# Kernel tuning notes

Measured on AMD Instinct MI355X. Metric: run time of the kernel, lower is better.

The kernel has to match this reference:

```python
import jax, jax.numpy as jnp
import numpy as np

B, C_IN, N = 64, 1, 8192
WIDTH, MODES, NLAYERS = 64, 16, 4


def setup_inputs() -> dict:
    key = jax.random.key(0)
    ks = jax.random.split(key, 10)
    scale = 1.0 / (WIDTH * WIDTH)
    inp = {
        "x": jax.random.normal(ks[0], (B, C_IN, N), dtype=jnp.float32),
        # lifting p: Linear(2, width)
        "p_w": jax.random.normal(ks[1], (WIDTH, 2), dtype=jnp.float32) * 0.5,
        "p_b": jax.random.normal(ks[2], (WIDTH,), dtype=jnp.float32) * 0.1,
        # 4 spectral conv weights, complex stored as real/imag (uniform like torch.rand cfloat)
        "sc_wr": scale * jax.random.uniform(ks[3], (NLAYERS, WIDTH, WIDTH, MODES), dtype=jnp.float32),
        "sc_wi": scale * jax.random.uniform(ks[4], (NLAYERS, WIDTH, WIDTH, MODES), dtype=jnp.float32),
        # 4 pointwise (1x1) conv weights/biases
        "w_w": jax.random.normal(ks[5], (NLAYERS, WIDTH, WIDTH), dtype=jnp.float32) / np.sqrt(WIDTH),
        "w_b": jax.random.normal(ks[6], (NLAYERS, WIDTH), dtype=jnp.float32) * 0.1,
        # projection q: Linear(width, 1)
        "q_w": jax.random.normal(ks[7], (1, WIDTH), dtype=jnp.float32) / np.sqrt(WIDTH),
        "q_b": jax.random.normal(ks[8], (1,), dtype=jnp.float32) * 0.1,
    }
    return inp


def spectral_conv(x, wr, wi, n):
    # x: [b, i, n] real; weights complex [i, o, modes]
    x_ft = jnp.fft.rfft(x, axis=-1)                      # [b, i, n//2+1] complex
    w = (wr + 1j * wi).astype(jnp.complex64)
    out_modes = jnp.einsum('bix,iox->box', x_ft[:, :, :MODES], w)
    out_ft = jnp.zeros((x.shape[0], w.shape[1], n // 2 + 1), dtype=jnp.complex64)
    out_ft = out_ft.at[:, :, :MODES].set(out_modes)
    return jnp.fft.irfft(out_ft, n=n, axis=-1)


def reference(x, p_w, p_b, sc_wr, sc_wi, w_w, w_b, q_w, q_b):
    b, _, n = x.shape
    grid = jnp.broadcast_to(jnp.linspace(0.0, 1.0, n, dtype=jnp.float32)[None, None, :], (b, 1, n))
    h = jnp.concatenate([x, grid], axis=1)               # [b, 2, n]
    # lifting: Linear over channel dim
    h = jnp.einsum('bcn,wc->bwn', h, p_w) + p_b[None, :, None]
    for l in range(NLAYERS):
        x1 = spectral_conv(h, sc_wr[l], sc_wi[l], n)
        x2 = jnp.einsum('bin,oi->bon', h, w_w[l]) + w_b[l][None, :, None]
        h = jax.nn.gelu(x1 + x2, approximate=False)
    out = jnp.einsum('bwn,ow->bon', h, q_w) + q_b[None, :, None]  # [b, 1, n]
    return out
```

## Files before the change

### kernel.cpp

```cpp
#include <hip/hip_runtime.h>
#include <math.h>


typedef _Float16 f16;
typedef _Float16 f16x2 __attribute__((ext_vector_type(2)));
typedef _Float16 f16x4 __attribute__((ext_vector_type(4)));
typedef _Float16 f16x8 __attribute__((ext_vector_type(8)));
typedef float    f32x2 __attribute__((ext_vector_type(2)));
typedef float    f32x4 __attribute__((ext_vector_type(4)));
typedef unsigned int u32;

#define BB 64
#define NN 8192

#define HT_S 64
#define HO_S 136
#define WS_S 72
#define MS_S 40
#define BI_S 40
#define BF_S 136

__device__ __forceinline__ int ht_swz(int n) { return ((n & 7) ^ ((n >> 3) & 7)) << 3; }

__device__ __forceinline__ float gelu_f(float v) {
    float x  = v * 0.70710678118654752f;
    float ax = fabsf(x);
    float t  = __builtin_amdgcn_rcpf(fmaf(0.3275911f, ax, 1.0f));
    float p  = fmaf(1.061405429f, t, -1.453152027f);
    p = fmaf(p, t, 1.421413741f);
    p = fmaf(p, t, -0.284496736f);
    p = fmaf(p, t, 0.254829592f);
    p = p * t;
    float e  = __expf(-x * x);
    float er = fmaf(-p, e, 1.0f);
    er = copysignf(er, x);
    return 0.5f * fmaf(v, er, v);
}

__global__ __launch_bounds__(256) void fill_basis(f16* __restrict__ basF,
                                                  f16* __restrict__ basI,
                                                  const float* __restrict__ w_w,
                                                  f16* __restrict__ Wh,
                                                  float* __restrict__ Sz) {
    int n = blockIdx.x * 256 + threadIdx.x;
    f16 row[32];
#pragma unroll
    for (int k = 0; k < 16; ++k) {
        float s, c;
        sincospif((float)(k * n) * (1.0f / 4096.0f), &s, &c);
        basF[k * NN + n]        = (f16)c;
        basF[(16 + k) * NN + n] = (f16)(-s);
        row[2 * k]     = (f16)c;
        row[2 * k + 1] = (f16)s;
    }
#pragma unroll
    for (int q = 0; q < 4; ++q) *(f16x8*)&basI[n * 32 + 8 * q] = *(f16x8*)&row[8 * q];
    Wh[n]        = (f16)w_w[n];
    Wh[n + 8192] = (f16)w_w[n + 8192];
    f32x4* S4 = (f32x4*)Sz;
    f32x4 z = {0.f, 0.f, 0.f, 0.f};
#pragma unroll
    for (int u = 0; u < 4; ++u) S4[n * 4 + u] = z;
}

__global__ __launch_bounds__(1024) void mode_mix(float* __restrict__ S,
                                                 const float* __restrict__ wr,
                                                 const float* __restrict__ wi,
                                                 f16* __restrict__ Mph) {
    int b = blockIdx.x, t = threadIdx.x;
    __shared__ float Ss[32 * 66];
    if (t < 512) {
        f32x4 v = *(const f32x4*)&S[b * 2048 + t * 4];
        int rw = t >> 4, cl = (t & 15) * 4;
#pragma unroll
        for (int e = 0; e < 4; ++e) Ss[rw * 66 + cl + e] = v[e];
    }
    __syncthreads();
    *(f32x2*)&S[b * 2048 + t * 2] = (f32x2){0.f, 0.f};

    int o = t >> 4, k = t & 15;
    const float* wrp = wr + o * 16 + k;
    const float* wip = wi + o * 16 + k;
    float ar = 0.f, ai = 0.f;
#pragma unroll 8
    for (int i = 0; i < 64; ++i) {
        float sr = Ss[k * 66 + i], si = Ss[(16 + k) * 66 + i];
        float wrv = wrp[i * 1024];
        float wiv = wip[i * 1024];
        ar = fmaf(sr, wrv, ar); ar = fmaf(-si, wiv, ar);
        ai = fmaf(sr, wiv, ai); ai = fmaf(si, wrv, ai);
    }
    float sc = (k == 0 ? 1.0f : 2.0f) * (1.0f / 8192.0f);
    f16x2 outv = { (f16)(sc * ar), (f16)(-sc * ai) };
    *(f16x2*)&Mph[b * 2048 + o * 32 + 2 * k] = outv;
}

__device__ __forceinline__ void dft_accum(const f16* Hout, const f16* BasF,
                                          f32x4 sacc[2], int lane, int wv) {
    int q = lane >> 4, l15 = lane & 15;
    int o = (wv << 4) + l15;
#pragma unroll
    for (int ks = 0; ks < 4; ++ks) {
        f16x8 bh = *(const f16x8*)&Hout[o * HO_S + ks * 32 + q * 8];
#pragma unroll
        for (int mt = 0; mt < 2; ++mt) {
            f16x8 af = *(const f16x8*)&BasF[(mt * 16 + l15) * BF_S + ks * 32 + q * 8];
            sacc[mt] = __builtin_amdgcn_mfma_f32_16x16x32_f16(af, bh, sacc[mt], 0, 0, 0);
        }
    }
}

__device__ __forceinline__ void dft_flush(const f32x4 sacc[2], float* __restrict__ S,
                                          int b, int lane, int wv) {
    int q = lane >> 4, l15 = lane & 15;
#pragma unroll
    for (int mt = 0; mt < 2; ++mt)
#pragma unroll
        for (int r = 0; r < 4; ++r)
            atomicAdd(&S[(b * 32 + mt * 16 + q * 4 + r) * 64 + (wv << 4) + l15],
                      sacc[mt][r]);
}

__global__ __launch_bounds__(256, 3) void lift_kernel(const float* __restrict__ x,
                                                      const float* __restrict__ p_w,
                                                      const float* __restrict__ p_b,
                                                      f16* __restrict__ h,
                                                      const f16* __restrict__ basF_g,
                                                      float* __restrict__ S) {
    __shared__ f16 Hout[64 * HO_S];
    __shared__ f16 BasF[32 * BF_S];
    int t = threadIdx.x;
    int b = blockIdx.x >> 5;
    int g = blockIdx.x & 31;
    int lane = t & 63, wv = t >> 6;
    int ns = (t & 15) << 3;

    float w0[4], w1[4], pb[4];
#pragma unroll
    for (int r = 0; r < 4; ++r) {
        int o = (t >> 4) + 16 * r;
        w0[r] = p_w[2 * o]; w1[r] = p_w[2 * o + 1]; pb[r] = p_b[o];
    }

    f32x4 X[2][2];
#pragma unroll
    for (int tile = 0; tile < 2; ++tile) {
        int n0 = ((g << 1) + tile) << 7;
        X[tile][0] = *(const f32x4*)&x[(b << 13) + n0 + ns];
        X[tile][1] = *(const f32x4*)&x[(b << 13) + n0 + ns + 4];
    }

    f32x4 sacc[2] = {{0.f,0.f,0.f,0.f},{0.f,0.f,0.f,0.f}};
#pragma unroll
    for (int tile = 0; tile < 2; ++tile) {
        int n0 = ((g << 1) + tile) << 7;
#pragma unroll
        for (int r = 0; r < 4; ++r) {
            int o = (t >> 4) + 16 * r;
            f16 vals[8];
#pragma unroll
            for (int j = 0; j < 8; ++j) {
                int n = n0 + ns + j;
                float xv = X[tile][j >> 2][j & 3];
                vals[j] = (f16)(w0[r] * xv + w1[r] * ((float)n * (1.0f / 8191.0f)) + pb[r]);
            }
            *(f16x8*)&Hout[o * HO_S + ns] = *(f16x8*)vals;
            *(f16x8*)(h + (((size_t)(b * 64 + o)) << 13) + n0 + ns) = *(f16x8*)vals;
        }
#pragma unroll
        for (int u = 0; u < 2; ++u) {
            int km = t >> 3, nn = (t & 7) * 16 + u * 8;
            *(f16x8*)&BasF[km * BF_S + nn] = *(const f16x8*)&basF_g[km * NN + n0 + nn];
        }
        __syncthreads();
        dft_accum(Hout, BasF, sacc, lane, wv);
        if (tile == 0) __syncthreads();
    }
    dft_flush(sacc, S, b, lane, wv);
}

template <int DO_DFT>
__global__ __launch_bounds__(256, 3) void layer_kernel(f16* __restrict__ h,
                                                       const f16* __restrict__ Wl_h,
                                                       const float* __restrict__ bl,
                                                       const f16* __restrict__ Mph,
                                                       const f16* __restrict__ basF_g,
                                                       const f16* __restrict__ basI_g,
                                                       float* __restrict__ S,
                                                       const float* __restrict__ q_w,
                                                       const float* __restrict__ q_b,
                                                       float* __restrict__ out) {
    __shared__ __align__(16) char pool[16384 + 9216];
    f16* Ht   = (f16*)pool;
    f16* Ws   = (f16*)(pool + 16384);
    f16* Hout = (f16*)pool;
    __shared__ f16 Ms2[64 * MS_S];
    __shared__ f16 BasI[128 * BI_S];
    __shared__ f16 BasF[32 * BF_S];
    __shared__ float bls[64];
    int t = threadIdx.x;
    int b = blockIdx.x >> 5;
    int g = blockIdx.x & 31;
    f16* hbase = h + (((size_t)(b * 64)) << 13);
    int lane = t & 63, wv = t >> 6;
    int q = lane >> 4, l15 = lane & 15;

    if (t >= 128) {
        int t2 = t - 128;
        {
            int o = t2 & 63, hs = (t2 >> 6) * 32;
            const f16* src = Wl_h + o * 64 + hs;
            f16* dst = &Ws[o * WS_S + hs];
#pragma unroll
            for (int u = 0; u < 4; ++u) *(f16x8*)&dst[8 * u] = *(const f16x8*)&src[8 * u];
        }
        {
            int o = t2 >> 1, seg = (t2 & 1) * 16;
            const f16* src = Mph + b * 2048 + o * 32 + seg;
            f16* dst = &Ms2[o * MS_S + seg];
            *(f16x8*)&dst[0] = *(const f16x8*)&src[0];
            *(f16x8*)&dst[8] = *(const f16x8*)&src[8];
        }
    }
    if (t < 64) bls[t] = bl[t];

    f16x8 Bw[4][2], Bm[4];
    f32x4 sacc[2] = {{0.f,0.f,0.f,0.f},{0.f,0.f,0.f,0.f}};

    for (int tile = 0; tile < 2; ++tile) {
        int n0 = ((g << 1) + tile) << 7;
        f16* hbt = hbase + n0;

        if (t < 128) {
            int ig = t >> 4, nb = t & 15;
            int i0 = ig << 3, ns = nb << 3;
            f16x8 R[8];
#pragma unroll
            for (int k = 0; k < 8; ++k)
                R[k] = *(const f16x8*)(hbt + ((size_t)(i0 + k) << 13) + ns);
            const u32* rd = (const u32*)R;
            int swz = nb & 7;
#pragma unroll
            for (int j = 0; j < 8; ++j) {
                u32 o[4] __attribute__((aligned(16)));
                u32 sel = (j & 1) ? 0x07060302u : 0x05040100u;
                int jd = j >> 1;
#pragma unroll
                for (int e = 0; e < 4; ++e)
                    o[e] = __builtin_amdgcn_perm(rd[(2 * e + 1) * 4 + jd],
                                                 rd[(2 * e) * 4 + jd], sel);
                int col = i0 ^ ((j ^ swz) << 3);
                *(f16x8*)&Ht[(ns + j) * HT_S + col] = *(const f16x8*)o;
            }
        } else {
            int t2 = t - 128;
            {
                const f16* src = basI_g + (size_t)(n0 + t2) * 32;
                f16* dst = &BasI[t2 * BI_S];
#pragma unroll
                for (int u = 0; u < 4; ++u) *(f16x8*)&dst[8 * u] = *(const f16x8*)&src[8 * u];
            }
            if (DO_DFT) {
                int km = t2 >> 2, seg = (t2 & 3) * 32;
                const f16* src = basF_g + km * NN + n0 + seg;
                f16* dst = &BasF[km * BF_S + seg];
#pragma unroll
                for (int u = 0; u < 4; ++u) *(f16x8*)&dst[8 * u] = *(const f16x8*)&src[8 * u];
            }
        }
        __syncthreads();

        if (tile == 0) {
#pragma unroll
            for (int ct = 0; ct < 4; ++ct) {
#pragma unroll
                for (int ks = 0; ks < 2; ++ks)
                    Bw[ct][ks] = *(const f16x8*)&Ws[(ct * 16 + l15) * WS_S + ks * 32 + q * 8];
                Bm[ct] = *(const f16x8*)&Ms2[(ct * 16 + l15) * MS_S + q * 8];
            }
        }

        f32x4 acc[4][2];
#pragma unroll
        for (int ct = 0; ct < 4; ++ct)
#pragma unroll
            for (int m = 0; m < 2; ++m) acc[ct][m] = (f32x4){0.f, 0.f, 0.f, 0.f};

#pragma unroll
        for (int mtl = 0; mtl < 2; ++mtl) {
            int nrow = (2 * wv + mtl) * 16 + l15;
            const f16* hrow = &Ht[nrow * HT_S];
            int g3 = ht_swz(nrow);
#pragma unroll
            for (int ks = 0; ks < 2; ++ks) {
                f16x8 Ah = *(const f16x8*)&hrow[(ks * 32 + q * 8) ^ g3];
#pragma unroll
                for (int ct = 0; ct < 4; ++ct)
                    acc[ct][mtl] = __builtin_amdgcn_mfma_f32_16x16x32_f16(
                        Ah, Bw[ct][ks], acc[ct][mtl], 0, 0, 0);
            }
            f16x8 Ab = *(const f16x8*)&BasI[nrow * BI_S + q * 8];
#pragma unroll
            for (int ct = 0; ct < 4; ++ct)
                acc[ct][mtl] = __builtin_amdgcn_mfma_f32_16x16x32_f16(
                    Ab, Bm[ct], acc[ct][mtl], 0, 0, 0);
        }

        float bv[4];
#pragma unroll
        for (int ct = 0; ct < 4; ++ct) bv[ct] = bls[ct * 16 + l15];

        if (DO_DFT) {
            __syncthreads();
#pragma unroll
            for (int ct = 0; ct < 4; ++ct) {
                int o = ct * 16 + l15;
#pragma unroll
                for (int mtl = 0; mtl < 2; ++mtl) {
                    int nbase = (2 * wv + mtl) * 16 + q * 4;
                    float gg[4];
#pragma unroll
                    for (int r = 0; r < 4; ++r)
                        gg[r] = gelu_f(acc[ct][mtl][r] + bv[ct]);
                    f16x2 lo = __builtin_bit_cast(f16x2, __builtin_amdgcn_cvt_pkrtz(gg[0], gg[1]));
                    f16x2 hi = __builtin_bit_cast(f16x2, __builtin_amdgcn_cvt_pkrtz(gg[2], gg[3]));
                    f16x4 pk = {lo[0], lo[1], hi[0], hi[1]};
                    *(f16x4*)&Hout[o * HO_S + nbase] = pk;
                }
            }
            __syncthreads();
#pragma unroll
            for (int r = 0; r < 4; ++r) {
                int o = (t >> 4) + 16 * r;
                int ns2 = (t & 15) << 3;
                *(f16x8*)(hbt + ((size_t)o << 13) + ns2) = *(f16x8*)&Hout[o * HO_S + ns2];
            }
            dft_accum(Hout, BasF, sacc, lane, wv);
        } else {
            float qv[4];
#pragma unroll
            for (int ct = 0; ct < 4; ++ct) qv[ct] = q_w[ct * 16 + l15];
            float part[2][4] = {{0.f,0.f,0.f,0.f},{0.f,0.f,0.f,0.f}};
#pragma unroll
            for (int ct = 0; ct < 4; ++ct)
#pragma unroll
                for (int mtl = 0; mtl < 2; ++mtl)
#pragma unroll
                    for (int r = 0; r < 4; ++r)
                        part[mtl][r] = fmaf(qv[ct],
                            gelu_f(acc[ct][mtl][r] + bv[ct]), part[mtl][r]);
#pragma unroll
            for (int mtl = 0; mtl < 2; ++mtl)
#pragma unroll
                for (int r = 0; r < 4; ++r) {
                    float s = part[mtl][r];
#pragma unroll
                    for (int m = 1; m < 16; m <<= 1)
                        s += __shfl_xor(s, m, 64);
                    if (l15 == 0)
                        out[(b << 13) + n0 + (2 * wv + mtl) * 16 + q * 4 + r] =
                            s + q_b[0];
                }
        }
        if (tile == 0) __syncthreads();
    }
    if (DO_DFT) dft_flush(sacc, S, b, lane, wv);
}

extern "C" void kernel_launch(void* const* d_in, const int* in_sizes, int n_in,
                              void* d_out, int out_size, void* d_ws, size_t ws_size,
                              hipStream_t stream) {
    const float* x     = (const float*)d_in[0];
    const float* p_w   = (const float*)d_in[1];
    const float* p_b   = (const float*)d_in[2];
    const float* sc_wr = (const float*)d_in[3];
    const float* sc_wi = (const float*)d_in[4];
    const float* w_w   = (const float*)d_in[5];
    const float* w_b   = (const float*)d_in[6];
    const float* q_w   = (const float*)d_in[7];
    const float* q_b   = (const float*)d_in[8];
    float* out = (float*)d_out;

    char* ws = (char*)d_ws;
    f16*   h    = (f16*)ws;
    float* S    = (float*)(ws + 67108864ull);
    f16*   Mph  = (f16*)(ws + 67633152ull);
    f16*   basF = (f16*)(ws + 67895296ull);
    f16*   basI = (f16*)(ws + 68419584ull);
    f16*   Wh   = (f16*)(ws + 68943872ull);

    hipLaunchKernelGGL(fill_basis, dim3(NN / 256), dim3(256), 0, stream,
                       basF, basI, w_w, Wh, S);
    hipLaunchKernelGGL(lift_kernel, dim3(BB * 32), dim3(256), 0, stream,
                       x, p_w, p_b, h, basF, S);
    for (int l = 0; l < 4; ++l) {
        hipLaunchKernelGGL(mode_mix, dim3(BB), dim3(1024), 0, stream,
                           S, sc_wr + l * 65536, sc_wi + l * 65536, Mph);
        if (l < 3) {
            hipLaunchKernelGGL((layer_kernel<1>), dim3(BB * 32), dim3(256), 0, stream,
                               h, Wh + l * 4096, w_b + l * 64, Mph, basF, basI, S,
                               q_w, q_b, out);
        } else {
            hipLaunchKernelGGL((layer_kernel<0>), dim3(BB * 32), dim3(256), 0, stream,
                               h, Wh + l * 4096, w_b + l * 64, Mph, basF, basI, S,
                               q_w, q_b, out);
        }
    }
}
```

Baseline: 267.1 us.

## Software-pipeline layer tiles, drop basis/weight LDS staging, read fragments from global

Restructures the layer kernel into an explicitly unrolled two-tile pipeline. The second tile's h rows and inverse-basis fragments are prefetched into registers while the first tile computes, and all 256 threads now share the transpose. Weights, spectral mode coefficients and DFT basis fragments are loaded directly from global memory into MFMA operands instead of being staged through shared memory, which shrinks LDS use and removes barriers. The risks are higher register pressure under launch_bounds(256,3) and uncoalesced global fragment loads that depend on cache hits.

```diff
diff --git a/kernel.cpp b/kernel.cpp
--- a/kernel.cpp
+++ b/kernel.cpp
@@ -15,10 +15,6 @@
 
 #define HT_S 64
 #define HO_S 136
-#define WS_S 72
-#define MS_S 40
-#define BI_S 40
-#define BF_S 136
 
 __device__ __forceinline__ int ht_swz(int n) { return ((n & 7) ^ ((n >> 3) & 7)) << 3; }
 
@@ -95,8 +91,8 @@
     *(f16x2*)&Mph[b * 2048 + o * 32 + 2 * k] = outv;
 }
 
-__device__ __forceinline__ void dft_accum(const f16* Hout, const f16* BasF,
-                                          f32x4 sacc[2], int lane, int wv) {
+__device__ __forceinline__ void dft_accum_g(const f16* Hout, const f16* __restrict__ basF_g,
+                                            int n0, f32x4 sacc[2], int lane, int wv) {
     int q = lane >> 4, l15 = lane & 15;
     int o = (wv << 4) + l15;
 #pragma unroll
@@ -104,7 +100,7 @@
         f16x8 bh = *(const f16x8*)&Hout[o * HO_S + ks * 32 + q * 8];
 #pragma unroll
         for (int mt = 0; mt < 2; ++mt) {
-            f16x8 af = *(const f16x8*)&BasF[(mt * 16 + l15) * BF_S + ks * 32 + q * 8];
+            f16x8 af = *(const f16x8*)&basF_g[(mt * 16 + l15) * NN + n0 + ks * 32 + q * 8];
             sacc[mt] = __builtin_amdgcn_mfma_f32_16x16x32_f16(af, bh, sacc[mt], 0, 0, 0);
         }
     }
@@ -128,7 +124,6 @@
                                                       const f16* __restrict__ basF_g,
                                                       float* __restrict__ S) {
     __shared__ f16 Hout[64 * HO_S];
-    __shared__ f16 BasF[32 * BF_S];
     int t = threadIdx.x;
     int b = blockIdx.x >> 5;
     int g = blockIdx.x & 31;
@@ -167,13 +162,8 @@
             *(f16x8*)&Hout[o * HO_S + ns] = *(f16x8*)vals;
             *(f16x8*)(h + (((size_t)(b * 64 + o)) << 13) + n0 + ns) = *(f16x8*)vals;
         }
-#pragma unroll
-        for (int u = 0; u < 2; ++u) {
-            int km = t >> 3, nn = (t & 7) * 16 + u * 8;
-            *(f16x8*)&BasF[km * BF_S + nn] = *(const f16x8*)&basF_g[km * NN + n0 + nn];
-        }
-        __syncthreads();
-        dft_accum(Hout, BasF, sacc, lane, wv);
+        __syncthreads();
+        dft_accum_g(Hout, basF_g, n0, sacc, lane, wv);
         if (tile == 0) __syncthreads();
     }
     dft_flush(sacc, S, b, lane, wv);
@@ -190,13 +180,8 @@
                                                        const float* __restrict__ q_w,
                                                        const float* __restrict__ q_b,
                                                        float* __restrict__ out) {
-    __shared__ __align__(16) char pool[16384 + 9216];
-    f16* Ht   = (f16*)pool;
-    f16* Ws   = (f16*)(pool + 16384);
-    f16* Hout = (f16*)pool;
-    __shared__ f16 Ms2[64 * MS_S];
-    __shared__ f16 BasI[128 * BI_S];
-    __shared__ f16 BasF[32 * BF_S];
+    __shared__ __align__(16) f16 Ht[128 * HT_S];
+    __shared__ __align__(16) f16 Hout[DO_DFT ? 64 * HO_S : 8];
     __shared__ float bls[64];
     int t = threadIdx.x;
     int b = blockIdx.x >> 5;
@@ -204,167 +189,236 @@
     f16* hbase = h + (((size_t)(b * 64)) << 13);
     int lane = t & 63, wv = t >> 6;
     int q = lane >> 4, l15 = lane & 15;
-
-    if (t >= 128) {
-        int t2 = t - 128;
+    int blk = t >> 1, half = t & 1;
+    int ig = blk >> 4, nb = blk & 15;
+    int i0 = ig << 3, nst = nb << 3;
+    int swz = nb & 7;
+    int n0_0 = (g << 1) << 7, n0_1 = ((g << 1) + 1) << 7;
+    f16* hbt0 = hbase + n0_0;
+    f16* hbt1 = hbase + n0_1;
+
+    f16x8 Bw[4][2], Bm[4];
+#pragma unroll
+    for (int ct = 0; ct < 4; ++ct) {
+#pragma unroll
+        for (int ks = 0; ks < 2; ++ks)
+            Bw[ct][ks] = *(const f16x8*)&Wl_h[(ct * 16 + l15) * 64 + ks * 32 + q * 8];
+        Bm[ct] = *(const f16x8*)&Mph[b * 2048 + (ct * 16 + l15) * 32 + q * 8];
+    }
+    if (t < 64) bls[t] = bl[t];
+
+    f16x8 R0[4];
+#pragma unroll
+    for (int k = 0; k < 4; ++k)
+        R0[k] = *(const f16x8*)(hbt0 + ((size_t)(i0 + half * 4 + k) << 13) + nst);
+    f16x8 Ab0[2];
+#pragma unroll
+    for (int mtl = 0; mtl < 2; ++mtl)
+        Ab0[mtl] = *(const f16x8*)&basI_g[(size_t)(n0_0 + (2 * wv + mtl) * 16 + l15) * 32 + q * 8];
+    {
+        const u32* rd = (const u32*)R0;
+#pragma unroll
+        for (int j = 0; j < 8; ++j) {
+            u32 sel = (j & 1) ? 0x07060302u : 0x05040100u;
+            int jd = j >> 1;
+            u32 oo[2] __attribute__((aligned(8)));
+            oo[0] = __builtin_amdgcn_perm(rd[4 + jd],  rd[jd],      sel);
+            oo[1] = __builtin_amdgcn_perm(rd[12 + jd], rd[8 + jd],  sel);
+            int col = (i0 ^ ((j ^ swz) << 3)) + half * 4;
+            *(f16x4*)&Ht[(nst + j) * HT_S + col] = *(const f16x4*)oo;
+        }
+    }
+    __syncthreads();
+
+    f16x8 R1[4];
+#pragma unroll
+    for (int k = 0; k < 4; ++k)
+        R1[k] = *(const f16x8*)(hbt1 + ((size_t)(i0 + half * 4 + k) << 13) + nst);
+    f16x8 Ab1[2];
+#pragma unroll
+    for (int mtl = 0; mtl < 2; ++mtl)
+        Ab1[mtl] = *(const f16x8*)&basI_g[(size_t)(n0_1 + (2 * wv + mtl) * 16 + l15) * 32 + q * 8];
+
+    float bv[4];
+#pragma unroll
+    for (int ct = 0; ct < 4; ++ct) bv[ct] = bls[ct * 16 + l15];
+
+    f32x4 sacc[2] = {{0.f,0.f,0.f,0.f},{0.f,0.f,0.f,0.f}};
+
+    f32x4 acc[4][2];
+#pragma unroll
+    for (int ct = 0; ct < 4; ++ct)
+#pragma unroll
+        for (int m = 0; m < 2; ++m) acc[ct][m] = (f32x4){0.f, 0.f, 0.f, 0.f};
+#pragma unroll
+    for (int mtl = 0; mtl < 2; ++mtl) {
+        int nrow = (2 * wv + mtl) * 16 + l15;
+        const f16* hrow = &Ht[nrow * HT_S];
+        int g3 = ht_swz(nrow);
+#pragma unroll
+        for (int ks = 0; ks < 2; ++ks) {
+            f16x8 Ah = *(const f16x8*)&hrow[(ks * 32 + q * 8) ^ g3];
+#pragma unroll
+            for (int ct = 0; ct < 4; ++ct)
+                acc[ct][mtl] = __builtin_amdgcn_mfma_f32_16x16x32_f16(
+                    Ah, Bw[ct][ks], acc[ct][mtl], 0, 0, 0);
+        }
+#pragma unroll
+        for (int ct = 0; ct < 4; ++ct)
+            acc[ct][mtl] = __builtin_amdgcn_mfma_f32_16x16x32_f16(
+                Ab0[mtl], Bm[ct], acc[ct][mtl], 0, 0, 0);
+    }
+
+    if (DO_DFT) {
+#pragma unroll
+        for (int ct = 0; ct < 4; ++ct) {
+            int o = ct * 16 + l15;
+#pragma unroll
+            for (int mtl = 0; mtl < 2; ++mtl) {
+                int nbase = (2 * wv + mtl) * 16 + q * 4;
+                float gg[4];
+#pragma unroll
+                for (int r = 0; r < 4; ++r)
+                    gg[r] = gelu_f(acc[ct][mtl][r] + bv[ct]);
+                f16x2 lo = __builtin_bit_cast(f16x2, __builtin_amdgcn_cvt_pkrtz(gg[0], gg[1]));
+                f16x2 hi = __builtin_bit_cast(f16x2, __builtin_amdgcn_cvt_pkrtz(gg[2], gg[3]));
+                f16x4 pk = {lo[0], lo[1], hi[0], hi[1]};
+                *(f16x4*)&Hout[o * HO_S + nbase] = pk;
+            }
+        }
+        __syncthreads();
+#pragma unroll
+        for (int r = 0; r < 4; ++r) {
+            int o = (t >> 4) + 16 * r;
+            int ns2 = (t & 15) << 3;
+            *(f16x8*)(hbt0 + ((size_t)o << 13) + ns2) = *(f16x8*)&Hout[o * HO_S + ns2];
+        }
         {
-            int o = t2 & 63, hs = (t2 >> 6) * 32;
-            const f16* src = Wl_h + o * 64 + hs;
-            f16* dst = &Ws[o * WS_S + hs];
-#pragma unroll
-            for (int u = 0; u < 4; ++u) *(f16x8*)&dst[8 * u] = *(const f16x8*)&src[8 * u];
-        }
-        {
-            int o = t2 >> 1, seg = (t2 & 1) * 16;
-            const f16* src = Mph + b * 2048 + o * 32 + seg;
-            f16* dst = &Ms2[o * MS_S + seg];
-            *(f16x8*)&dst[0] = *(const f16x8*)&src[0];
-            *(f16x8*)&dst[8] = *(const f16x8*)&src[8];
-        }
-    }
-    if (t < 64) bls[t] = bl[t];
-
-    f16x8 Bw[4][2], Bm[4];
-    f32x4 sacc[2] = {{0.f,0.f,0.f,0.f},{0.f,0.f,0.f,0.f}};
-
-    for (int tile = 0; tile < 2; ++tile) {
-        int n0 = ((g << 1) + tile) << 7;
-        f16* hbt = hbase + n0;
-
-        if (t < 128) {
-            int ig = t >> 4, nb = t & 15;
-            int i0 = ig << 3, ns = nb << 3;
-            f16x8 R[8];
-#pragma unroll
-            for (int k = 0; k < 8; ++k)
-                R[k] = *(const f16x8*)(hbt + ((size_t)(i0 + k) << 13) + ns);
-            const u32* rd = (const u32*)R;
-            int swz = nb & 7;
+            const u32* rd = (const u32*)R1;
 #pragma unroll
             for (int j = 0; j < 8; ++j) {
-                u32 o[4] __attribute__((aligned(16)));
                 u32 sel = (j & 1) ? 0x07060302u : 0x05040100u;
                 int jd = j >> 1;
-#pragma unroll
-                for (int e = 0; e < 4; ++e)
-                    o[e] = __builtin_amdgcn_perm(rd[(2 * e + 1) * 4 + jd],
-                                                 rd[(2 * e) * 4 + jd], sel);
-                int col = i0 ^ ((j ^ swz) << 3);
-                *(f16x8*)&Ht[(ns + j) * HT_S + col] = *(const f16x8*)o;
-            }
-        } else {
-            int t2 = t - 128;
-            {
-                const f16* src = basI_g + (size_t)(n0 + t2) * 32;
-                f16* dst = &BasI[t2 * BI_S];
-#pragma unroll
-                for (int u = 0; u < 4; ++u) *(f16x8*)&dst[8 * u] = *(const f16x8*)&src[8 * u];
-            }
-            if (DO_DFT) {
-                int km = t2 >> 2, seg = (t2 & 3) * 32;
-                const f16* src = basF_g + km * NN + n0 + seg;
-                f16* dst = &BasF[km * BF_S + seg];
-#pragma unroll
-                for (int u = 0; u < 4; ++u) *(f16x8*)&dst[8 * u] = *(const f16x8*)&src[8 * u];
-            }
-        }
-        __syncthreads();
-
-        if (tile == 0) {
-#pragma unroll
-            for (int ct = 0; ct < 4; ++ct) {
-#pragma unroll
-                for (int ks = 0; ks < 2; ++ks)
-                    Bw[ct][ks] = *(const f16x8*)&Ws[(ct * 16 + l15) * WS_S + ks * 32 + q * 8];
-                Bm[ct] = *(const f16x8*)&Ms2[(ct * 16 + l15) * MS_S + q * 8];
-            }
-        }
-
-        f32x4 acc[4][2];
+                u32 oo[2] __attribute__((aligned(8)));
+                oo[0] = __builtin_amdgcn_perm(rd[4 + jd],  rd[jd],     sel);
+                oo[1] = __builtin_amdgcn_perm(rd[12 + jd], rd[8 + jd], sel);
+                int col = (i0 ^ ((j ^ swz) << 3)) + half * 4;
+                *(f16x4*)&Ht[(nst + j) * HT_S + col] = *(const f16x4*)oo;
+            }
+        }
+        dft_accum_g(Hout, basF_g, n0_0, sacc, lane, wv);
+        __syncthreads();
+    } else {
+        float qv[4];
+#pragma unroll
+        for (int ct = 0; ct < 4; ++ct) qv[ct] = q_w[ct * 16 + l15];
+        float part[2][4] = {{0.f,0.f,0.f,0.f},{0.f,0.f,0.f,0.f}};
 #pragma unroll
         for (int ct = 0; ct < 4; ++ct)
 #pragma unroll
-            for (int m = 0; m < 2; ++m) acc[ct][m] = (f32x4){0.f, 0.f, 0.f, 0.f};
-
-#pragma unroll
-        for (int mtl = 0; mtl < 2; ++mtl) {
-            int nrow = (2 * wv + mtl) * 16 + l15;
-            const f16* hrow = &Ht[nrow * HT_S];
-            int g3 = ht_swz(nrow);
-#pragma unroll
-            for (int ks = 0; ks < 2; ++ks) {
-                f16x8 Ah = *(const f16x8*)&hrow[(ks * 32 + q * 8) ^ g3];
-#pragma unroll
-                for (int ct = 0; ct < 4; ++ct)
-                    acc[ct][mtl] = __builtin_amdgcn_mfma_f32_16x16x32_f16(
-                        Ah, Bw[ct][ks], acc[ct][mtl], 0, 0, 0);
-            }
-            f16x8 Ab = *(const f16x8*)&BasI[nrow * BI_S + q * 8];
+            for (int mtl = 0; mtl < 2; ++mtl)
+#pragma unroll
+                for (int r = 0; r < 4; ++r)
+                    part[mtl][r] = fmaf(qv[ct], gelu_f(acc[ct][mtl][r] + bv[ct]), part[mtl][r]);
+#pragma unroll
+        for (int mtl = 0; mtl < 2; ++mtl)
+#pragma unroll
+            for (int r = 0; r < 4; ++r) {
+                float s = part[mtl][r];
+#pragma unroll
+                for (int m = 1; m < 16; m <<= 1) s += __shfl_xor(s, m, 64);
+                if (l15 == 0)
+                    out[(b << 13) + n0_0 + (2 * wv + mtl) * 16 + q * 4 + r] = s + q_b[0];
+            }
+        __syncthreads();
+        {
+            const u32* rd = (const u32*)R1;
+#pragma unroll
+            for (int j = 0; j < 8; ++j) {
+                u32 sel = (j & 1) ? 0x07060302u : 0x05040100u;
+                int jd = j >> 1;
+                u32 oo[2] __attribute__((aligned(8)));
+                oo[0] = __builtin_amdgcn_perm(rd[4 + jd],  rd[jd],     sel);
+                oo[1] = __builtin_amdgcn_perm(rd[12 + jd], rd[8 + jd], sel);
+                int col = (i0 ^ ((j ^ swz) << 3)) + half * 4;
+                *(f16x4*)&Ht[(nst + j) * HT_S + col] = *(const f16x4*)oo;
+            }
+        }
+        __syncthreads();
+    }
+
+#pragma unroll
+    for (int ct = 0; ct < 4; ++ct)
+#pragma unroll
+        for (int m = 0; m < 2; ++m) acc[ct][m] = (f32x4){0.f, 0.f, 0.f, 0.f};
+#pragma unroll
+    for (int mtl = 0; mtl < 2; ++mtl) {
+        int nrow = (2 * wv + mtl) * 16 + l15;
+        const f16* hrow = &Ht[nrow * HT_S];
+        int g3 = ht_swz(nrow);
+#pragma unroll
+        for (int ks = 0; ks < 2; ++ks) {
+            f16x8 Ah = *(const f16x8*)&hrow[(ks * 32 + q * 8) ^ g3];
 #pragma unroll
             for (int ct = 0; ct < 4; ++ct)
                 acc[ct][mtl] = __builtin_amdgcn_mfma_f32_16x16x32_f16(
-                    Ab, Bm[ct], acc[ct][mtl], 0, 0, 0);
-        }
-
-        float bv[4];
-#pragma unroll
-        for (int ct = 0; ct < 4; ++ct) bv[ct] = bls[ct * 16 + l15];
-
-        if (DO_DFT) {
-            __syncthreads();
-#pragma unroll
-            for (int ct = 0; ct < 4; ++ct) {
-                int o = ct * 16 + l15;
-#pragma unroll
-                for (int mtl = 0; mtl < 2; ++mtl) {
-                    int nbase = (2 * wv + mtl) * 16 + q * 4;
-                    float gg[4];
-#pragma unroll
-                    for (int r = 0; r < 4; ++r)
-                        gg[r] = gelu_f(acc[ct][mtl][r] + bv[ct]);
-                    f16x2 lo = __builtin_bit_cast(f16x2, __builtin_amdgcn_cvt_pkrtz(gg[0], gg[1]));
-                    f16x2 hi = __builtin_bit_cast(f16x2, __builtin_amdgcn_cvt_pkrtz(gg[2], gg[3]));
-                    f16x4 pk = {lo[0], lo[1], hi[0], hi[1]};
-                    *(f16x4*)&Hout[o * HO_S + nbase] = pk;
-                }
-            }
-            __syncthreads();
+                    Ah, Bw[ct][ks], acc[ct][mtl], 0, 0, 0);
+        }
+#pragma unroll
+        for (int ct = 0; ct < 4; ++ct)
+            acc[ct][mtl] = __builtin_amdgcn_mfma_f32_16x16x32_f16(
+                Ab1[mtl], Bm[ct], acc[ct][mtl], 0, 0, 0);
+    }
+
+    if (DO_DFT) {
+#pragma unroll
+        for (int ct = 0; ct < 4; ++ct) {
+            int o = ct * 16 + l15;
+#pragma unroll
+            for (int mtl = 0; mtl < 2; ++mtl) {
+                int nbase = (2 * wv + mtl) * 16 + q * 4;
+                float gg[4];
+#pragma unroll
+                for (int r = 0; r < 4; ++r)
+                    gg[r] = gelu_f(acc[ct][mtl][r] + bv[ct]);
+                f16x2 lo = __builtin_bit_cast(f16x2, __builtin_amdgcn_cvt_pkrtz(gg[0], gg[1]));
+                f16x2 hi = __builtin_bit_cast(f16x2, __builtin_amdgcn_cvt_pkrtz(gg[2], gg[3]));
+                f16x4 pk = {lo[0], lo[1], hi[0], hi[1]};
+                *(f16x4*)&Hout[o * HO_S + nbase] = pk;
+            }
+        }
+        __syncthreads();
+#pragma unroll
+        for (int r = 0; r < 4; ++r) {
+            int o = (t >> 4) + 16 * r;
+            int ns2 = (t & 15) << 3;
+            *(f16x8*)(hbt1 + ((size_t)o << 13) + ns2) = *(f16x8*)&Hout[o * HO_S + ns2];
+        }
+        dft_accum_g(Hout, basF_g, n0_1, sacc, lane, wv);
+        dft_flush(sacc, S, b, lane, wv);
+    } else {
+        float qv[4];
+#pragma unroll
+        for (int ct = 0; ct < 4; ++ct) qv[ct] = q_w[ct * 16 + l15];
+        float part[2][4] = {{0.f,0.f,0.f,0.f},{0.f,0.f,0.f,0.f}};
+#pragma unroll
+        for (int ct = 0; ct < 4; ++ct)
+#pragma unroll
+            for (int mtl = 0; mtl < 2; ++mtl)
+#pragma unroll
+                for (int r = 0; r < 4; ++r)
+                    part[mtl][r] = fmaf(qv[ct], gelu_f(acc[ct][mtl][r] + bv[ct]), part[mtl][r]);
+#pragma unroll
+        for (int mtl = 0; mtl < 2; ++mtl)
 #pragma unroll
             for (int r = 0; r < 4; ++r) {
-                int o = (t >> 4) + 16 * r;
-                int ns2 = (t & 15) << 3;
-                *(f16x8*)(hbt + ((size_t)o << 13) + ns2) = *(f16x8*)&Hout[o * HO_S + ns2];
-            }
-            dft_accum(Hout, BasF, sacc, lane, wv);
-        } else {
-            float qv[4];
-#pragma unroll
-            for (int ct = 0; ct < 4; ++ct) qv[ct] = q_w[ct * 16 + l15];
-            float part[2][4] = {{0.f,0.f,0.f,0.f},{0.f,0.f,0.f,0.f}};
-#pragma unroll
-            for (int ct = 0; ct < 4; ++ct)
-#pragma unroll
-                for (int mtl = 0; mtl < 2; ++mtl)
-#pragma unroll
-                    for (int r = 0; r < 4; ++r)
-                        part[mtl][r] = fmaf(qv[ct],
-                            gelu_f(acc[ct][mtl][r] + bv[ct]), part[mtl][r]);
-#pragma unroll
-            for (int mtl = 0; mtl < 2; ++mtl)
-#pragma unroll
-                for (int r = 0; r < 4; ++r) {
-                    float s = part[mtl][r];
-#pragma unroll
-                    for (int m = 1; m < 16; m <<= 1)
-                        s += __shfl_xor(s, m, 64);
-                    if (l15 == 0)
-                        out[(b << 13) + n0 + (2 * wv + mtl) * 16 + q * 4 + r] =
-                            s + q_b[0];
-                }
-        }
-        if (tile == 0) __syncthreads();
-    }
-    if (DO_DFT) dft_flush(sacc, S, b, lane, wv);
+                float s = part[mtl][r];
+#pragma unroll
+                for (int m = 1; m < 16; m <<= 1) s += __shfl_xor(s, m, 64);
+                if (l15 == 0)
+                    out[(b << 13) + n0_1 + (2 * wv + mtl) * 16 + q * 4 + r] = s + q_b[0];
+            }
+    }
 }
 
 extern "C" void kernel_launch(void* const* d_in, const int* in_sizes, int n_in,
```

Measured after the change: 288.8 us. 1.08x slower.

## Pipeline h tile loads across four tiles per block and read bases from global

Applied to the files above, without the earlier changes.

Each layer block now processes four 128-column tiles instead of two, halving the grid, and prefetches the next tile's h into registers while computing the current one. All 256 threads share the transpose into LDS. Weights, mode-mix matrix, bias and basis fragments are read straight from global into registers instead of being staged in LDS, which shrinks LDS use and removes barriers. The aim is to hide global latency and cut sync and staging overhead, at the cost of fewer blocks, more register pressure and uncached global basis reads.

```diff
diff --git a/kernel.cpp b/kernel.cpp
--- a/kernel.cpp
+++ b/kernel.cpp
@@ -15,9 +15,6 @@
 
 #define HT_S 64
 #define HO_S 136
-#define WS_S 72
-#define MS_S 40
-#define BI_S 40
 #define BF_S 136
 
 __device__ __forceinline__ int ht_swz(int n) { return ((n & 7) ^ ((n >> 3) & 7)) << 3; }
@@ -37,6 +34,21 @@
     return 0.5f * fmaf(v, er, v);
 }
 
+__device__ __forceinline__ void perm_to_Ht(const f16x8* Rr, f16* Ht,
+                                           int i0, int nst, int swz, int half) {
+    const u32* rd = (const u32*)Rr;
+#pragma unroll
+    for (int j = 0; j < 8; ++j) {
+        u32 sel = (j & 1) ? 0x07060302u : 0x05040100u;
+        int jd = j >> 1;
+        u32 oo[2] __attribute__((aligned(8)));
+        oo[0] = __builtin_amdgcn_perm(rd[4 + jd],  rd[jd],     sel);
+        oo[1] = __builtin_amdgcn_perm(rd[12 + jd], rd[8 + jd], sel);
+        int col = (i0 ^ ((j ^ swz) << 3)) + half * 4;
+        *(f16x4*)&Ht[(nst + j) * HT_S + col] = *(const f16x4*)oo;
+    }
+}
+
 __global__ __launch_bounds__(256) void fill_basis(f16* __restrict__ basF,
                                                   f16* __restrict__ basI,
                                                   const float* __restrict__ w_w,
@@ -105,6 +117,21 @@
 #pragma unroll
         for (int mt = 0; mt < 2; ++mt) {
             f16x8 af = *(const f16x8*)&BasF[(mt * 16 + l15) * BF_S + ks * 32 + q * 8];
+            sacc[mt] = __builtin_amdgcn_mfma_f32_16x16x32_f16(af, bh, sacc[mt], 0, 0, 0);
+        }
+    }
+}
+
+__device__ __forceinline__ void dft_accum_g(const f16* Hout, const f16* __restrict__ basF_g,
+                                            int n0, f32x4 sacc[2], int lane, int wv) {
+    int q = lane >> 4, l15 = lane & 15;
+    int o = (wv << 4) + l15;
+#pragma unroll
+    for (int ks = 0; ks < 4; ++ks) {
+        f16x8 bh = *(const f16x8*)&Hout[o * HO_S + ks * 32 + q * 8];
+#pragma unroll
+        for (int mt = 0; mt < 2; ++mt) {
+            f16x8 af = *(const f16x8*)&basF_g[(mt * 16 + l15) * NN + n0 + ks * 32 + q * 8];
             sacc[mt] = __builtin_amdgcn_mfma_f32_16x16x32_f16(af, bh, sacc[mt], 0, 0, 0);
         }
     }
@@ -190,102 +217,68 @@
                                                        const float* __restrict__ q_w,
                                                        const float* __restrict__ q_b,
                                                        float* __restrict__ out) {
-    __shared__ __align__(16) char pool[16384 + 9216];
-    f16* Ht   = (f16*)pool;
-    f16* Ws   = (f16*)(pool + 16384);
-    f16* Hout = (f16*)pool;
-    __shared__ f16 Ms2[64 * MS_S];
-    __shared__ f16 BasI[128 * BI_S];
-    __shared__ f16 BasF[32 * BF_S];
-    __shared__ float bls[64];
+    __shared__ __align__(16) f16 Ht[128 * HT_S];
+    __shared__ __align__(16) f16 Hout[DO_DFT ? 64 * HO_S : 8];
     int t = threadIdx.x;
-    int b = blockIdx.x >> 5;
-    int g = blockIdx.x & 31;
+    int b = blockIdx.x >> 4;
+    int g = blockIdx.x & 15;
     f16* hbase = h + (((size_t)(b * 64)) << 13);
     int lane = t & 63, wv = t >> 6;
     int q = lane >> 4, l15 = lane & 15;
-
-    if (t >= 128) {
-        int t2 = t - 128;
-        {
-            int o = t2 & 63, hs = (t2 >> 6) * 32;
-            const f16* src = Wl_h + o * 64 + hs;
-            f16* dst = &Ws[o * WS_S + hs];
-#pragma unroll
-            for (int u = 0; u < 4; ++u) *(f16x8*)&dst[8 * u] = *(const f16x8*)&src[8 * u];
-        }
-        {
-            int o = t2 >> 1, seg = (t2 & 1) * 16;
-            const f16* src = Mph + b * 2048 + o * 32 + seg;
-            f16* dst = &Ms2[o * MS_S + seg];
-            *(f16x8*)&dst[0] = *(const f16x8*)&src[0];
-            *(f16x8*)&dst[8] = *(const f16x8*)&src[8];
-        }
-    }
-    if (t < 64) bls[t] = bl[t];
+    int blk = t >> 1, half = t & 1;
+    int ig = blk >> 4, nb = blk & 15;
+    int i0 = ig << 3, nst = nb << 3;
+    int swz = nb & 7;
 
     f16x8 Bw[4][2], Bm[4];
+#pragma unroll
+    for (int ct = 0; ct < 4; ++ct) {
+#pragma unroll
+        for (int ks = 0; ks < 2; ++ks)
+            Bw[ct][ks] = *(const f16x8*)&Wl_h[(ct * 16 + l15) * 64 + ks * 32 + q * 8];
+        Bm[ct] = *(const f16x8*)&Mph[b * 2048 + (ct * 16 + l15) * 32 + q * 8];
+    }
+    float bv[4], qv[4];
+#pragma unroll
+    for (int ct = 0; ct < 4; ++ct) {
+        bv[ct] = bl[ct * 16 + l15];
+        if (!DO_DFT) qv[ct] = q_w[ct * 16 + l15];
+    }
+
+    f16x8 R[2][4];
+    {
+        const f16* hbt = hbase + ((g << 2) << 7);
+#pragma unroll
+        for (int kk = 0; kk < 4; ++kk)
+            R[0][kk] = *(const f16x8*)(hbt + ((size_t)(i0 + half * 4 + kk) << 13) + nst);
+        perm_to_Ht(R[0], Ht, i0, nst, swz, half);
+    }
+    __syncthreads();
+
     f32x4 sacc[2] = {{0.f,0.f,0.f,0.f},{0.f,0.f,0.f,0.f}};
 
-    for (int tile = 0; tile < 2; ++tile) {
-        int n0 = ((g << 1) + tile) << 7;
+#pragma unroll
+    for (int k = 0; k < 4; ++k) {
+        const int nxt = (k & 1) ^ 1;
+        const int n0 = ((g << 2) + k) << 7;
         f16* hbt = hbase + n0;
 
-        if (t < 128) {
-            int ig = t >> 4, nb = t & 15;
-            int i0 = ig << 3, ns = nb << 3;
-            f16x8 R[8];
-#pragma unroll
-            for (int k = 0; k < 8; ++k)
-                R[k] = *(const f16x8*)(hbt + ((size_t)(i0 + k) << 13) + ns);
-            const u32* rd = (const u32*)R;
-            int swz = nb & 7;
-#pragma unroll
-            for (int j = 0; j < 8; ++j) {
-                u32 o[4] __attribute__((aligned(16)));
-                u32 sel = (j & 1) ? 0x07060302u : 0x05040100u;
-                int jd = j >> 1;
-#pragma unroll
-                for (int e = 0; e < 4; ++e)
-                    o[e] = __builtin_amdgcn_perm(rd[(2 * e + 1) * 4 + jd],
-                                                 rd[(2 * e) * 4 + jd], sel);
-                int col = i0 ^ ((j ^ swz) << 3);
-                *(f16x8*)&Ht[(ns + j) * HT_S + col] = *(const f16x8*)o;
-            }
-        } else {
-            int t2 = t - 128;
-            {
-                const f16* src = basI_g + (size_t)(n0 + t2) * 32;
-                f16* dst = &BasI[t2 * BI_S];
-#pragma unroll
-                for (int u = 0; u < 4; ++u) *(f16x8*)&dst[8 * u] = *(const f16x8*)&src[8 * u];
-            }
-            if (DO_DFT) {
-                int km = t2 >> 2, seg = (t2 & 3) * 32;
-                const f16* src = basF_g + km * NN + n0 + seg;
-                f16* dst = &BasF[km * BF_S + seg];
-#pragma unroll
-                for (int u = 0; u < 4; ++u) *(f16x8*)&dst[8 * u] = *(const f16x8*)&src[8 * u];
-            }
-        }
-        __syncthreads();
-
-        if (tile == 0) {
-#pragma unroll
-            for (int ct = 0; ct < 4; ++ct) {
-#pragma unroll
-                for (int ks = 0; ks < 2; ++ks)
-                    Bw[ct][ks] = *(const f16x8*)&Ws[(ct * 16 + l15) * WS_S + ks * 32 + q * 8];
-                Bm[ct] = *(const f16x8*)&Ms2[(ct * 16 + l15) * MS_S + q * 8];
-            }
-        }
+        if (k < 3) {
+            const f16* hbtn = hbase + n0 + 128;
+#pragma unroll
+            for (int kk = 0; kk < 4; ++kk)
+                R[nxt][kk] = *(const f16x8*)(hbtn + ((size_t)(i0 + half * 4 + kk) << 13) + nst);
+        }
+        f16x8 Ab[2];
+#pragma unroll
+        for (int mtl = 0; mtl < 2; ++mtl)
+            Ab[mtl] = *(const f16x8*)&basI_g[(size_t)(n0 + (2 * wv + mtl) * 16 + l15) * 32 + q * 8];
 
         f32x4 acc[4][2];
 #pragma unroll
         for (int ct = 0; ct < 4; ++ct)
 #pragma unroll
             for (int m = 0; m < 2; ++m) acc[ct][m] = (f32x4){0.f, 0.f, 0.f, 0.f};
-
 #pragma unroll
         for (int mtl = 0; mtl < 2; ++mtl) {
             int nrow = (2 * wv + mtl) * 16 + l15;
@@ -299,19 +292,13 @@
                     acc[ct][mtl] = __builtin_amdgcn_mfma_f32_16x16x32_f16(
                         Ah, Bw[ct][ks], acc[ct][mtl], 0, 0, 0);
             }
-            f16x8 Ab = *(const f16x8*)&BasI[nrow * BI_S + q * 8];
 #pragma unroll
             for (int ct = 0; ct < 4; ++ct)
                 acc[ct][mtl] = __builtin_amdgcn_mfma_f32_16x16x32_f16(
-                    Ab, Bm[ct], acc[ct][mtl], 0, 0, 0);
-        }
-
-        float bv[4];
-#pragma unroll
-        for (int ct = 0; ct < 4; ++ct) bv[ct] = bls[ct * 16 + l15];
+                    Ab[mtl], Bm[ct], acc[ct][mtl], 0, 0, 0);
+        }
 
         if (DO_DFT) {
-            __syncthreads();
 #pragma unroll
             for (int ct = 0; ct < 4; ++ct) {
                 int o = ct * 16 + l15;
@@ -335,11 +322,12 @@
                 int ns2 = (t & 15) << 3;
                 *(f16x8*)(hbt + ((size_t)o << 13) + ns2) = *(f16x8*)&Hout[o * HO_S + ns2];
             }
-            dft_accum(Hout, BasF, sacc, lane, wv);
+            dft_accum_g(Hout, basF_g, n0, sacc, lane, wv);
+            if (k < 3) {
+                perm_to_Ht(R[nxt], Ht, i0, nst, swz, half);
+                __syncthreads();
+            }
         } else {
-            float qv[4];
-#pragma unroll
-            for (int ct = 0; ct < 4; ++ct) qv[ct] = q_w[ct * 16 + l15];
             float part[2][4] = {{0.f,0.f,0.f,0.f},{0.f,0.f,0.f,0.f}};
 #pragma unroll
             for (int ct = 0; ct < 4; ++ct)
@@ -347,22 +335,23 @@
                 for (int mtl = 0; mtl < 2; ++mtl)
 #pragma unroll
                     for (int r = 0; r < 4; ++r)
-                        part[mtl][r] = fmaf(qv[ct],
-                            gelu_f(acc[ct][mtl][r] + bv[ct]), part[mtl][r]);
+                        part[mtl][r] = fmaf(qv[ct], gelu_f(acc[ct][mtl][r] + bv[ct]), part[mtl][r]);
 #pragma unroll
             for (int mtl = 0; mtl < 2; ++mtl)
 #pragma unroll
                 for (int r = 0; r < 4; ++r) {
                     float s = part[mtl][r];
 #pragma unroll
-                    for (int m = 1; m < 16; m <<= 1)
-                        s += __shfl_xor(s, m, 64);
+                    for (int m = 1; m < 16; m <<= 1) s += __shfl_xor(s, m, 64);
                     if (l15 == 0)
-                        out[(b << 13) + n0 + (2 * wv + mtl) * 16 + q * 4 + r] =
-                            s + q_b[0];
+                        out[(b << 13) + n0 + (2 * wv + mtl) * 16 + q * 4 + r] = s + q_b[0];
                 }
-        }
-        if (tile == 0) __syncthreads();
+            if (k < 3) {
+                __syncthreads();
+                perm_to_Ht(R[nxt], Ht, i0, nst, swz, half);
+                __syncthreads();
+            }
+        }
     }
     if (DO_DFT) dft_flush(sacc, S, b, lane, wv);
 }
@@ -397,11 +386,11 @@
         hipLaunchKernelGGL(mode_mix, dim3(BB), dim3(1024), 0, stream,
                            S, sc_wr + l * 65536, sc_wi + l * 65536, Mph);
         if (l < 3) {
-            hipLaunchKernelGGL((layer_kernel<1>), dim3(BB * 32), dim3(256), 0, stream,
+            hipLaunchKernelGGL((layer_kernel<1>), dim3(BB * 16), dim3(256), 0, stream,
                                h, Wh + l * 4096, w_b + l * 64, Mph, basF, basI, S,
                                q_w, q_b, out);
         } else {
-            hipLaunchKernelGGL((layer_kernel<0>), dim3(BB * 32), dim3(256), 0, stream,
+            hipLaunchKernelGGL((layer_kernel<0>), dim3(BB * 16), dim3(256), 0, stream,
                                h, Wh + l * 4096, w_b + l * 64, Mph, basF, basI, S,
                                q_w, q_b, out);
         }
```

After: 288.0 us. 1.08x slower.
